# Optimization experiments

Measured on AMD Instinct MI355X. Metric: run time of the kernel, lower is better.

## Reference

```python
import jax, jax.numpy as jnp
import numpy as np


def setup_inputs() -> dict:
    key = jax.random.key(0)
    k1, k2, k3 = jax.random.split(key, 3)
    x = jax.random.normal(k1, (16, 128, 128, 64), dtype=jnp.float32)
    kernel = jax.random.normal(k2, (3, 3, 64, 128), dtype=jnp.float32) * 0.05
    bias = jax.random.normal(k3, (128,), dtype=jnp.float32) * 0.05
    return {"x": x, "kernel": kernel, "bias": bias}


def reference(x, kernel, bias):
    # Faithful to myconv2d: extract_patches (stride 1, rate 1, SAME) followed by
    # per-out-channel multiply+reduce over the flattened (kh*kw*cin) patch axis,
    # which is mathematically a stride-1 SAME conv2d. Expressed as a direct conv.
    out = jax.lax.conv_general_dilated(
        x, kernel,
        window_strides=(1, 1),
        padding="SAME",
        dimension_numbers=("NHWC", "HWIO", "NHWC"),
    )
    return out + bias  # bias broadcast over channel dim, as in call()
```

## Files before the change

### kernel.cpp

```cpp
#include <hip/hip_runtime.h>


#define HH 128
#define WW 128
#define CIN 64
#define COUT 128

typedef __attribute__((ext_vector_type(8))) short v8s;
typedef __attribute__((ext_vector_type(4))) float v4f;

#define ROW_CHUNKS 1040
#define WS_NEEDED  (9u * CIN * COUT * 2u)

static __device__ __forceinline__ unsigned short f2bf(float f) {
    unsigned int u = __float_as_uint(f);
    unsigned int r = (u + 0x7fffu + ((u >> 16) & 1u)) >> 16;
    return (unsigned short)r;
}

__global__ __launch_bounds__(256) void cvt_w(const float* __restrict__ wgt,
                                             unsigned short* __restrict__ wt) {
    int idx = blockIdx.x * 256 + threadIdx.x;
    if (idx >= 9 * CIN * COUT) return;
    int co  = idx & (COUT - 1);
    int ci  = (idx >> 7) & (CIN - 1);
    int tap = idx >> 13;
    wt[(tap * COUT + co) * CIN + ci] = f2bf(wgt[idx]);
}

__global__ __launch_bounds__(256, 3) void conv_mfma(
    const float* __restrict__ x,
    const unsigned short* __restrict__ wt,
    const float* __restrict__ bias,
    float* __restrict__ out) {
    __shared__ v8s smem[3 * ROW_CHUNKS];

    int bid = blockIdx.x;
    int logical = ((bid & 7) << 8) | (bid >> 3);
    int h = logical & (HH - 1);
    int n = logical >> 7;

    int tid  = threadIdx.x;
    int lane = tid & 63;
    int wid  = tid >> 6;
    int wi = wid >> 1;
    int wj = wid & 1;
    int l15  = lane & 15;
    int quad = lane >> 4;
    int pixelL = wi * 64 + l15;

    if (tid < 48) {
        int row = tid >> 4, k = tid & 15;
        int c = (k < 8) ? k : (1024 + k);
        smem[row * ROW_CHUNKS + c] = (v8s)(short)0;
    }

    #pragma unroll
    for (int dh = 0; dh < 3; ++dh) {
        int ih = h + dh - 1;
        if (ih < 0 || ih >= HH) continue;
        const float* rowf = x + ((size_t)(n * HH + ih)) * WW * CIN;
        #pragma unroll
        for (int k = 0; k < 4; ++k) {
            int c = 8 + tid + (k << 8);
            const float* p = rowf + (size_t)(c - 8) * 8;
            float4 a = *(const float4*)p;
            float4 b = *(const float4*)(p + 4);
            v8s ch;
            ch[0] = (short)f2bf(a.x); ch[1] = (short)f2bf(a.y);
            ch[2] = (short)f2bf(a.z); ch[3] = (short)f2bf(a.w);
            ch[4] = (short)f2bf(b.x); ch[5] = (short)f2bf(b.y);
            ch[6] = (short)f2bf(b.z); ch[7] = (short)f2bf(b.w);
            int cp = c ^ ((c >> 3) & 7);
            smem[dh * ROW_CHUNKS + cp] = ch;
        }
    }
    __syncthreads();

    v4f acc[4][4];
    #pragma unroll
    for (int i = 0; i < 4; ++i)
        #pragma unroll
        for (int j = 0; j < 4; ++j) acc[i][j] = (v4f)0.f;

    #pragma unroll
    for (int dh = 0; dh < 3; ++dh) {
        int ih = h + dh - 1;
        if (ih < 0 || ih >= HH) continue;
        const v8s* srow = smem + dh * ROW_CHUNKS;
        #pragma unroll
        for (int dw = 0; dw < 3; ++dw) {
            const unsigned short* wtap = wt + (dh * 3 + dw) * COUT * CIN;
            #pragma unroll
            for (int kc = 0; kc < 2; ++kc) {
                v8s bfrag[4];
                #pragma unroll
                for (int t = 0; t < 4; ++t) {
                    int co = wj * 64 + t * 16 + l15;
                    bfrag[t] = *(const v8s*)(wtap + co * CIN + kc * 32 + quad * 8);
                }
                v8s afrag[4];
                #pragma unroll
                for (int t = 0; t < 4; ++t) {
                    int pl = pixelL + t * 16 + dw;
                    int c  = pl * 8 + kc * 4 + quad;
                    afrag[t] = srow[c ^ (pl & 7)];
                }
                #pragma unroll
                for (int ti = 0; ti < 4; ++ti)
                    #pragma unroll
                    for (int tj = 0; tj < 4; ++tj)
                        acc[ti][tj] = __builtin_amdgcn_mfma_f32_16x16x32_bf16(
                            afrag[ti], bfrag[tj], acc[ti][tj], 0, 0, 0);
            }
        }
    }

    float bv[4];
    #pragma unroll
    for (int tj = 0; tj < 4; ++tj) bv[tj] = bias[wj * 64 + tj * 16 + l15];

    float* orow = out + ((size_t)(n * HH + h)) * WW * COUT;
    #pragma unroll
    for (int ti = 0; ti < 4; ++ti) {
        #pragma unroll
        for (int r = 0; r < 4; ++r) {
            int p = wi * 64 + ti * 16 + quad * 4 + r;
            float* op = orow + (size_t)p * COUT + wj * 64 + l15;
            #pragma unroll
            for (int tj = 0; tj < 4; ++tj)
                op[tj * 16] = acc[ti][tj][r] + bv[tj];
        }
    }
}

__global__ __launch_bounds__(256) void conv3x3_direct(
    const float* __restrict__ x, const float* __restrict__ wgt,
    const float* __restrict__ bias, float* __restrict__ out) {
    int idx = blockIdx.x * 256 + threadIdx.x;
    int co = idx & (COUT - 1);
    int w  = (idx >> 7) & (WW - 1);
    int h  = (idx >> 14) & (HH - 1);
    int n  = idx >> 21;
    float acc = bias[co];
    #pragma unroll
    for (int kh = 0; kh < 3; ++kh) {
        int ih = h + kh - 1;
        if (ih < 0 || ih >= HH) continue;
        #pragma unroll
        for (int kw = 0; kw < 3; ++kw) {
            int iw = w + kw - 1;
            if (iw < 0 || iw >= WW) continue;
            const float* xp = x + (((size_t)(n * HH + ih) * WW + iw) * CIN);
            const float* wp = wgt + ((size_t)((kh * 3 + kw) * CIN)) * COUT + co;
            #pragma unroll 8
            for (int ci = 0; ci < CIN; ++ci)
                acc = fmaf(xp[ci], wp[(size_t)ci * COUT], acc);
        }
    }
    out[idx] = acc;
}

extern "C" void kernel_launch(void* const* d_in, const int* in_sizes, int n_in,
                              void* d_out, int out_size, void* d_ws, size_t ws_size,
                              hipStream_t stream) {
    const float* x    = (const float*)d_in[0];
    const float* wgt  = (const float*)d_in[1];
    const float* bias = (const float*)d_in[2];
    float* out = (float*)d_out;

    if (ws_size < (size_t)WS_NEEDED) {
        int blocks = (out_size + 255) / 256;
        conv3x3_direct<<<blocks, 256, 0, stream>>>(x, wgt, bias, out);
        return;
    }

    unsigned short* wt = (unsigned short*)d_ws;
    cvt_w<<<(9 * CIN * COUT + 255) / 256, 256, 0, stream>>>(wgt, wt);
    conv_mfma<<<16 * HH, 256, 0, stream>>>(x, wt, bias, out);
}
```

Before: 256.0 us.

## Software-pipeline weight fragment loads and zero-fill halo rows to drop branches

Boundary input rows are now zero-filled in shared memory rather than skipped. This lets the main loop run all 18 tap/k-chunk steps without per-row branches, flattened into one unrolled loop. Weight fragments for the next step are prefetched from global memory into a second register set while the current step's MFMAs run, and A-fragment LDS reads are interleaved with the MFMA groups to hide latency. The cost is more registers for the double-buffered B fragments, and edge rows now do MFMAs on zeros.

```diff
diff --git a/kernel.cpp b/kernel.cpp
--- a/kernel.cpp
+++ b/kernel.cpp
@@ -58,21 +58,28 @@
     #pragma unroll
     for (int dh = 0; dh < 3; ++dh) {
         int ih = h + dh - 1;
-        if (ih < 0 || ih >= HH) continue;
-        const float* rowf = x + ((size_t)(n * HH + ih)) * WW * CIN;
-        #pragma unroll
-        for (int k = 0; k < 4; ++k) {
-            int c = 8 + tid + (k << 8);
-            const float* p = rowf + (size_t)(c - 8) * 8;
-            float4 a = *(const float4*)p;
-            float4 b = *(const float4*)(p + 4);
-            v8s ch;
-            ch[0] = (short)f2bf(a.x); ch[1] = (short)f2bf(a.y);
-            ch[2] = (short)f2bf(a.z); ch[3] = (short)f2bf(a.w);
-            ch[4] = (short)f2bf(b.x); ch[5] = (short)f2bf(b.y);
-            ch[6] = (short)f2bf(b.z); ch[7] = (short)f2bf(b.w);
-            int cp = c ^ ((c >> 3) & 7);
-            smem[dh * ROW_CHUNKS + cp] = ch;
+        v8s* dst = smem + dh * ROW_CHUNKS;
+        if (ih >= 0 && ih < HH) {
+            const float* rowf = x + ((size_t)(n * HH + ih)) * WW * CIN;
+            #pragma unroll
+            for (int k = 0; k < 4; ++k) {
+                int c = 8 + tid + (k << 8);
+                const float* p = rowf + (size_t)(c - 8) * 8;
+                float4 a = *(const float4*)p;
+                float4 b = *(const float4*)(p + 4);
+                v8s ch;
+                ch[0] = (short)f2bf(a.x); ch[1] = (short)f2bf(a.y);
+                ch[2] = (short)f2bf(a.z); ch[3] = (short)f2bf(a.w);
+                ch[4] = (short)f2bf(b.x); ch[5] = (short)f2bf(b.y);
+                ch[6] = (short)f2bf(b.z); ch[7] = (short)f2bf(b.w);
+                dst[c ^ ((c >> 3) & 7)] = ch;
+            }
+        } else {
+            #pragma unroll
+            for (int k = 0; k < 4; ++k) {
+                int c = 8 + tid + (k << 8);
+                dst[c ^ ((c >> 3) & 7)] = (v8s)(short)0;
+            }
         }
     }
     __syncthreads();
@@ -83,36 +90,58 @@
         #pragma unroll
         for (int j = 0; j < 4; ++j) acc[i][j] = (v4f)0.f;
 
-    #pragma unroll
-    for (int dh = 0; dh < 3; ++dh) {
-        int ih = h + dh - 1;
-        if (ih < 0 || ih >= HH) continue;
+    const unsigned short* wlane = wt + (wj * 64 + l15) * CIN + quad * 8;
+    int abase = pixelL * 8 + quad;
+
+    v8s bcur[4], bnxt[4];
+    #pragma unroll
+    for (int t = 0; t < 4; ++t)
+        bcur[t] = *(const v8s*)(wlane + t * 16 * CIN);
+
+    #pragma unroll
+    for (int s = 0; s < 18; ++s) {
+        const int tap = s >> 1;
+        const int dh  = tap / 3;
+        const int dw  = tap % 3;
+        const int kc  = s & 1;
+
+        if (s < 17) {
+            const int tapn = (s + 1) >> 1;
+            const int kcn  = (s + 1) & 1;
+            const unsigned short* wp =
+                wlane + tapn * (COUT * CIN) + kcn * 32;
+            #pragma unroll
+            for (int t = 0; t < 4; ++t)
+                bnxt[t] = *(const v8s*)(wp + t * 16 * CIN);
+        }
+
         const v8s* srow = smem + dh * ROW_CHUNKS;
-        #pragma unroll
-        for (int dw = 0; dw < 3; ++dw) {
-            const unsigned short* wtap = wt + (dh * 3 + dw) * COUT * CIN;
-            #pragma unroll
-            for (int kc = 0; kc < 2; ++kc) {
-                v8s bfrag[4];
-                #pragma unroll
-                for (int t = 0; t < 4; ++t) {
-                    int co = wj * 64 + t * 16 + l15;
-                    bfrag[t] = *(const v8s*)(wtap + co * CIN + kc * 32 + quad * 8);
-                }
-                v8s afrag[4];
-                #pragma unroll
-                for (int t = 0; t < 4; ++t) {
-                    int pl = pixelL + t * 16 + dw;
-                    int c  = pl * 8 + kc * 4 + quad;
-                    afrag[t] = srow[c ^ (pl & 7)];
-                }
-                #pragma unroll
-                for (int ti = 0; ti < 4; ++ti)
-                    #pragma unroll
-                    for (int tj = 0; tj < 4; ++tj)
-                        acc[ti][tj] = __builtin_amdgcn_mfma_f32_16x16x32_bf16(
-                            afrag[ti], bfrag[tj], acc[ti][tj], 0, 0, 0);
-            }
+        const int sw = (pixelL + dw) & 7;
+
+        v8s a0 = srow[(abase + (0 * 16 + dw) * 8 + kc * 4) ^ sw];
+        v8s a1 = srow[(abase + (1 * 16 + dw) * 8 + kc * 4) ^ sw];
+        #pragma unroll
+        for (int tj = 0; tj < 4; ++tj)
+            acc[0][tj] = __builtin_amdgcn_mfma_f32_16x16x32_bf16(
+                a0, bcur[tj], acc[0][tj], 0, 0, 0);
+        v8s a2 = srow[(abase + (2 * 16 + dw) * 8 + kc * 4) ^ sw];
+        #pragma unroll
+        for (int tj = 0; tj < 4; ++tj)
+            acc[1][tj] = __builtin_amdgcn_mfma_f32_16x16x32_bf16(
+                a1, bcur[tj], acc[1][tj], 0, 0, 0);
+        v8s a3 = srow[(abase + (3 * 16 + dw) * 8 + kc * 4) ^ sw];
+        #pragma unroll
+        for (int tj = 0; tj < 4; ++tj)
+            acc[2][tj] = __builtin_amdgcn_mfma_f32_16x16x32_bf16(
+                a2, bcur[tj], acc[2][tj], 0, 0, 0);
+        #pragma unroll
+        for (int tj = 0; tj < 4; ++tj)
+            acc[3][tj] = __builtin_amdgcn_mfma_f32_16x16x32_bf16(
+                a3, bcur[tj], acc[3][tj], 0, 0, 0);
+
+        if (s < 17) {
+            #pragma unroll
+            for (int t = 0; t < 4; ++t) bcur[t] = bnxt[t];
         }
     }
 
```

Result: faster. 248.0 us (-3.1%).
